# Kernel tuning notes

Measured on AMD Instinct MI355X. Metric: run time of the kernel, lower is better.

The kernel has to match this reference:

```python
import jax, jax.numpy as jnp
import numpy as np

# Markonv (Markov convolution): for each window position p and filter n,
#   out[b, n, p] = sum_{l=0}^{K-1} sum_{i,j} x[b, i, p*s + l] * x[b, j, p*s + l + 1] * W[l, i, j, n]
# i.e. the sum over the window of bilinear channel->channel transition scores
# between adjacent sequence positions (log-likelihood of a first-order Markov
# chain when x is one-hot). Output length = ceil((L - K)/s), matching the
# original CUDA module.

B, C, L = 128, 4, 10000   # batch, channels (DNA alphabet), sequence length
K, N = 20, 128            # kernel_length, kernel_number
STRIDE = 1


def setup_inputs() -> dict:
    key = jax.random.key(0)
    k1, k2 = jax.random.split(key)
    x = jax.random.uniform(k1, (B, C, L), dtype=jnp.float32)          # soft one-hot sequence
    W = jax.random.uniform(k2, (K, C, C, N), dtype=jnp.float32)       # uniform(0,1) init as in module
    return {"x": x, "W": W, "stride": STRIDE}


def reference(x, W, stride):
    Bb, Cc, Ll = x.shape
    Kk, _, _, Nn = W.shape
    # Adjacent-position transition features: pair[b, i*C + j, t] = x[b,i,t] * x[b,j,t+1]
    pair = (x[:, :, None, :-1] * x[:, None, :, 1:]).reshape(Bb, Cc * Cc, Ll - 1)
    # Kernel as a 1D conv filter over the C*C transition channels: kern[n, i*C+j, l]
    kern = jnp.transpose(W, (3, 1, 2, 0)).reshape(Nn, Cc * Cc, Kk)
    # Valid conv of length-K window over L-1 transitions, stride s ->
    # output length floor((L-1-K)/s)+1 == ceil((L-K)/s).
    out = jax.lax.conv_general_dilated(
        pair, kern,
        window_strides=(stride,),
        padding='VALID',
        dimension_numbers=('NCH', 'OIH', 'NCH'),
    )
    return out  # [B, N, ceil((L-K)/stride)]
```

## Files before the change

### kernel.cpp

```cpp
#include <hip/hip_runtime.h>


#define B_    128
#define C_    4
#define L_    10000
#define K_    20
#define N_    128
#define P_    9980
#define MT    64
#define ROWS  (MT + K_ - 1)
#define TPG   13
#define GRPS  12
#define PSTR  24

typedef float  f32x16 __attribute__((ext_vector_type(16)));
typedef __bf16 bf16x8 __attribute__((ext_vector_type(8)));
typedef unsigned short u16x8 __attribute__((ext_vector_type(8)));

static __device__ __forceinline__ unsigned short f2bf(float f) {
  union { float f; unsigned u; } v; v.f = f;
  unsigned r = (v.u + 0x7fffu + ((v.u >> 16) & 1u)) >> 16;
  return (unsigned short)r;
}

__global__ void convW_kernel(const float* __restrict__ W,
                             unsigned short* __restrict__ Wb) {
  int idx = blockIdx.x * 256 + threadIdx.x;
  if (idx < K_ * N_ * 16) {
    int ij = idx & 15, n = (idx >> 4) & (N_ - 1), l = idx >> 11;
    Wb[idx] = f2bf(W[(l * 16 + ij) * N_ + n]);
  }
}

__launch_bounds__(256, 3)
__global__ void markonv_kernel(const float* __restrict__ x,
                               const unsigned short* __restrict__ Wb,
                               const float* __restrict__ Wf,
                               float* __restrict__ out,
                               int useGather) {
  __shared__ __align__(16) float xs[C_][MT + 24];
  __shared__ __align__(16) unsigned short pairLds[ROWS * PSTR];

  const int tid  = threadIdx.x;
  const int lane = tid & 63;
  const int wid  = tid >> 6;
  const int h    = lane >> 5;
  const int nl   = lane & 31;
  const int b    = blockIdx.y;
  const int grp  = blockIdx.x;

  bf16x8 bfr[K_];
  if (useGather) {
    #pragma unroll
    for (int l = 0; l < K_; ++l) {
      int n = wid * 32 + nl;
      u16x8 u;
      #pragma unroll
      for (int j = 0; j < 8; ++j)
        u[j] = f2bf(Wf[(l * 16 + 8 * h + j) * N_ + n]);
      bfr[l] = __builtin_bit_cast(bf16x8, u);
    }
  } else {
    #pragma unroll
    for (int l = 0; l < K_; ++l) {
      int n = wid * 32 + nl;
      bfr[l] = __builtin_bit_cast(bf16x8,
          *(const u16x8*)(Wb + ((l * N_ + n) * 16 + 8 * h)));
    }
  }

  const float* xrow = x + (size_t)(b * C_ + wid) * L_;

  #pragma unroll 1
  for (int it = 0; it < TPG; ++it) {
    const int tile = grp * TPG + it;
    const int t0   = tile * MT;

    __syncthreads();
    {
      int t = t0 + lane;
      xs[wid][lane] = (t < L_) ? xrow[t] : 0.f;
      if (lane < (ROWS + 1 - 64)) {
        int t2 = t0 + 64 + lane;
        xs[wid][64 + lane] = (t2 < L_) ? xrow[t2] : 0.f;
      }
    }
    __syncthreads();
    if (tid < 2 * ROWS) {
      int r = tid >> 1, half = tid & 1;
      float x0 = xs[2 * half + 0][r], x1 = xs[2 * half + 1][r];
      float y0 = xs[0][r + 1], y1 = xs[1][r + 1];
      float y2 = xs[2][r + 1], y3 = xs[3][r + 1];
      u16x8 u;
      u[0] = f2bf(x0 * y0); u[1] = f2bf(x0 * y1);
      u[2] = f2bf(x0 * y2); u[3] = f2bf(x0 * y3);
      u[4] = f2bf(x1 * y0); u[5] = f2bf(x1 * y1);
      u[6] = f2bf(x1 * y2); u[7] = f2bf(x1 * y3);
      *(u16x8*)&pairLds[r * PSTR + 8 * half] = u;
    }
    __syncthreads();

    f32x16 acc0, acc1;
    #pragma unroll
    for (int i = 0; i < 16; ++i) { acc0[i] = 0.f; acc1[i] = 0.f; }

    #pragma unroll
    for (int l = 0; l < K_; ++l) {
      bf16x8 p0 = __builtin_bit_cast(bf16x8,
          *(const u16x8*)&pairLds[(nl + l) * PSTR + 8 * h]);
      bf16x8 p1 = __builtin_bit_cast(bf16x8,
          *(const u16x8*)&pairLds[(32 + nl + l) * PSTR + 8 * h]);
      acc0 = __builtin_amdgcn_mfma_f32_32x32x16_bf16(bfr[l], p0, acc0, 0, 0, 0);
      acc1 = __builtin_amdgcn_mfma_f32_32x32x16_bf16(bfr[l], p1, acc1, 0, 0, 0);
    }

    float* base = out + (size_t)(b * N_ + wid * 32 + 4 * h) * P_;
    {
      int p = t0 + nl;
      if (p < P_) {
        #pragma unroll
        for (int r = 0; r < 16; ++r) {
          int m = (r & 3) + 8 * (r >> 2);
          __builtin_nontemporal_store(acc0[r], base + (size_t)m * P_ + p);
        }
      }
      int p2 = t0 + 32 + nl;
      if (p2 < P_) {
        #pragma unroll
        for (int r = 0; r < 16; ++r) {
          int m = (r & 3) + 8 * (r >> 2);
          __builtin_nontemporal_store(acc1[r], base + (size_t)m * P_ + p2);
        }
      }
    }
  }
}

extern "C" void kernel_launch(void* const* d_in, const int* in_sizes, int n_in,
                              void* d_out, int out_size, void* d_ws, size_t ws_size,
                              hipStream_t stream) {
  const float* x  = (const float*)d_in[0];
  const float* W  = (const float*)d_in[1];
  float* out      = (float*)d_out;

  const size_t wbBytes = (size_t)K_ * N_ * 16 * sizeof(unsigned short);
  int useGather = (ws_size < wbBytes || d_ws == nullptr) ? 1 : 0;
  unsigned short* Wb = (unsigned short*)d_ws;

  if (!useGather) {
    convW_kernel<<<dim3((K_ * N_ * 16 + 255) / 256), dim3(256), 0, stream>>>(W, Wb);
  }
  markonv_kernel<<<dim3(GRPS, B_), dim3(256), 0, stream>>>(x, Wb, W, out, useGather);
}
```

Measured before the change: 1.026 ms.

## Build pair features once per block span and drop per-tile barriers

Each block now loads the x values for its entire 12-tile span with float4 loads and computes the bf16 pair features into LDS once. The tile loop then runs MFMAs and stores without any __syncthreads. The gather flag becomes a template parameter and the two output stores per row are interleaved. This increases LDS use per block, which could affect occupancy.

```diff
diff --git a/kernel.cpp b/kernel.cpp
--- a/kernel.cpp
+++ b/kernel.cpp
@@ -8,9 +8,11 @@
 #define N_    128
 #define P_    9980
 #define MT    64
-#define ROWS  (MT + K_ - 1)
-#define TPG   13
-#define GRPS  12
+#define TPG   12
+#define GRPS  13
+#define SPAN  (TPG * MT)
+#define ROWS  (SPAN + K_ - 1)
+#define XSL   (ROWS + 1)
 #define PSTR  24
 
 typedef float  f32x16 __attribute__((ext_vector_type(16)));
@@ -32,13 +34,13 @@
   }
 }
 
+template <int USE_GATHER>
 __launch_bounds__(256, 3)
 __global__ void markonv_kernel(const float* __restrict__ x,
                                const unsigned short* __restrict__ Wb,
                                const float* __restrict__ Wf,
-                               float* __restrict__ out,
-                               int useGather) {
-  __shared__ __align__(16) float xs[C_][MT + 24];
+                               float* __restrict__ out) {
+  __shared__ __align__(16) float xs[C_][XSL + 4];
   __shared__ __align__(16) unsigned short pairLds[ROWS * PSTR];
 
   const int tid  = threadIdx.x;
@@ -48,9 +50,10 @@
   const int nl   = lane & 31;
   const int b    = blockIdx.y;
   const int grp  = blockIdx.x;
+  const int t0g  = grp * SPAN;
 
   bf16x8 bfr[K_];
-  if (useGather) {
+  if (USE_GATHER) {
     #pragma unroll
     for (int l = 0; l < K_; ++l) {
       int n = wid * 32 + nl;
@@ -69,69 +72,66 @@
     }
   }
 
-  const float* xrow = x + (size_t)(b * C_ + wid) * L_;
+  {
+    const float* xrow = x + (size_t)(b * C_ + wid) * L_;
+    #pragma unroll 1
+    for (int v = lane; v < XSL / 4; v += 64) {
+      int t = t0g + 4 * v;
+      float4 val;
+      if (t + 3 < L_) {
+        val = *(const float4*)(xrow + t);
+      } else {
+        val.x = (t + 0 < L_) ? xrow[t + 0] : 0.f;
+        val.y = (t + 1 < L_) ? xrow[t + 1] : 0.f;
+        val.z = (t + 2 < L_) ? xrow[t + 2] : 0.f;
+        val.w = (t + 3 < L_) ? xrow[t + 3] : 0.f;
+      }
+      *(float4*)&xs[wid][4 * v] = val;
+    }
+  }
+  __syncthreads();
+
+  #pragma unroll 1
+  for (int task = tid; task < ROWS * 2; task += 256) {
+    int r = task >> 1, half = task & 1;
+    float x0 = xs[2 * half + 0][r], x1 = xs[2 * half + 1][r];
+    float y0 = xs[0][r + 1], y1 = xs[1][r + 1];
+    float y2 = xs[2][r + 1], y3 = xs[3][r + 1];
+    u16x8 u;
+    u[0] = f2bf(x0 * y0); u[1] = f2bf(x0 * y1);
+    u[2] = f2bf(x0 * y2); u[3] = f2bf(x0 * y3);
+    u[4] = f2bf(x1 * y0); u[5] = f2bf(x1 * y1);
+    u[6] = f2bf(x1 * y2); u[7] = f2bf(x1 * y3);
+    *(u16x8*)&pairLds[r * PSTR + 8 * half] = u;
+  }
+  __syncthreads();
 
   #pragma unroll 1
   for (int it = 0; it < TPG; ++it) {
-    const int tile = grp * TPG + it;
-    const int t0   = tile * MT;
-
-    __syncthreads();
-    {
-      int t = t0 + lane;
-      xs[wid][lane] = (t < L_) ? xrow[t] : 0.f;
-      if (lane < (ROWS + 1 - 64)) {
-        int t2 = t0 + 64 + lane;
-        xs[wid][64 + lane] = (t2 < L_) ? xrow[t2] : 0.f;
-      }
-    }
-    __syncthreads();
-    if (tid < 2 * ROWS) {
-      int r = tid >> 1, half = tid & 1;
-      float x0 = xs[2 * half + 0][r], x1 = xs[2 * half + 1][r];
-      float y0 = xs[0][r + 1], y1 = xs[1][r + 1];
-      float y2 = xs[2][r + 1], y3 = xs[3][r + 1];
-      u16x8 u;
-      u[0] = f2bf(x0 * y0); u[1] = f2bf(x0 * y1);
-      u[2] = f2bf(x0 * y2); u[3] = f2bf(x0 * y3);
-      u[4] = f2bf(x1 * y0); u[5] = f2bf(x1 * y1);
-      u[6] = f2bf(x1 * y2); u[7] = f2bf(x1 * y3);
-      *(u16x8*)&pairLds[r * PSTR + 8 * half] = u;
-    }
-    __syncthreads();
-
+    const int t0 = t0g + it * MT;
     f32x16 acc0, acc1;
     #pragma unroll
     for (int i = 0; i < 16; ++i) { acc0[i] = 0.f; acc1[i] = 0.f; }
 
+    const int rbase = it * MT + nl;
     #pragma unroll
     for (int l = 0; l < K_; ++l) {
       bf16x8 p0 = __builtin_bit_cast(bf16x8,
-          *(const u16x8*)&pairLds[(nl + l) * PSTR + 8 * h]);
+          *(const u16x8*)&pairLds[(rbase + l) * PSTR + 8 * h]);
       bf16x8 p1 = __builtin_bit_cast(bf16x8,
-          *(const u16x8*)&pairLds[(32 + nl + l) * PSTR + 8 * h]);
+          *(const u16x8*)&pairLds[(rbase + 32 + l) * PSTR + 8 * h]);
       acc0 = __builtin_amdgcn_mfma_f32_32x32x16_bf16(bfr[l], p0, acc0, 0, 0, 0);
       acc1 = __builtin_amdgcn_mfma_f32_32x32x16_bf16(bfr[l], p1, acc1, 0, 0, 0);
     }
 
     float* base = out + (size_t)(b * N_ + wid * 32 + 4 * h) * P_;
-    {
-      int p = t0 + nl;
-      if (p < P_) {
-        #pragma unroll
-        for (int r = 0; r < 16; ++r) {
-          int m = (r & 3) + 8 * (r >> 2);
-          __builtin_nontemporal_store(acc0[r], base + (size_t)m * P_ + p);
-        }
-      }
-      int p2 = t0 + 32 + nl;
-      if (p2 < P_) {
-        #pragma unroll
-        for (int r = 0; r < 16; ++r) {
-          int m = (r & 3) + 8 * (r >> 2);
-          __builtin_nontemporal_store(acc1[r], base + (size_t)m * P_ + p2);
-        }
-      }
+    const int p = t0 + nl, p2 = t0 + 32 + nl;
+    #pragma unroll
+    for (int r = 0; r < 16; ++r) {
+      int m = (r & 3) + 8 * (r >> 2);
+      float* orow = base + (size_t)m * P_;
+      if (p < P_)  __builtin_nontemporal_store(acc0[r], orow + p);
+      if (p2 < P_) __builtin_nontemporal_store(acc1[r], orow + p2);
     }
   }
 }
@@ -149,6 +149,8 @@
 
   if (!useGather) {
     convW_kernel<<<dim3((K_ * N_ * 16 + 255) / 256), dim3(256), 0, stream>>>(W, Wb);
+    markonv_kernel<0><<<dim3(GRPS, B_), dim3(256), 0, stream>>>(x, Wb, W, out);
+  } else {
+    markonv_kernel<1><<<dim3(GRPS, B_), dim3(256), 0, stream>>>(x, Wb, W, out);
   }
-  markonv_kernel<<<dim3(GRPS, B_), dim3(256), 0, stream>>>(x, Wb, W, out, useGather);
 }
```

After: 911.6 us. -11.1%, faster.
